# Kernel optimization log

Measured on AMD Instinct MI355X. Metric: run time of the kernel, lower is better.

## Reference

```python
import jax, jax.numpy as jnp
import numpy as np
from jax import lax

N_HEADS = 12
HEAD_DIM = 64
ALPHA = 4.0  # spikingjelly surrogate.Sigmoid default alpha
EPS = 1e-5   # BatchNorm1d default eps

@jax.custom_vjp
def _heaviside(v):
    return (v >= 0.0).astype(v.dtype)

def _heaviside_fwd(v):
    return _heaviside(v), v

def _heaviside_bwd(v, g):
    sg = jax.nn.sigmoid(ALPHA * v)
    return (g * ALPHA * sg * (1.0 - sg),)

_heaviside.defvjp(_heaviside_fwd, _heaviside_bwd)

def if_node(x):
    """Multi-step IFNode (v_threshold=1, hard reset to 0), scan over leading T dim."""
    def step(v, xt):
        v = v + xt                      # integrate
        s = _heaviside(v - 1.0)         # fire
        v = (1.0 - s) * v               # hard reset: spiked neurons -> 0
        return v, s
    _, spikes = lax.scan(step, jnp.zeros_like(x[0]), x)
    return spikes

def bn1d(x):
    """Fresh (training-mode) BatchNorm1d over (T, S, D) with channels=S;
    affine weight=1, bias=0 at init, so pure normalization over axes (0,2)."""
    mean = x.mean(axis=(0, 2), keepdims=True)
    var = x.var(axis=(0, 2), keepdims=True)  # biased variance, as torch BN uses
    return (x - mean) * lax.rsqrt(var + EPS)

def setup_inputs() -> dict:
    key = jax.random.key(0)
    ks = jax.random.split(key, 5)
    T, S, D = 4, 2048, 768
    x = jax.random.normal(ks[0], (T, S, D), dtype=jnp.float32)
    scale = 0.02
    wq = jax.random.normal(ks[1], (D, D), dtype=jnp.float32) * scale
    wk = jax.random.normal(ks[2], (D, D), dtype=jnp.float32) * scale
    wv = jax.random.normal(ks[3], (D, D), dtype=jnp.float32) * scale
    wo = jax.random.normal(ks[4], (D, D), dtype=jnp.float32) * scale
    return {"x": x, "wq": wq, "wk": wk, "wv": wv, "wo": wo, "cur_pos": S}

def reference(x, wq, wk, wv, wo, cur_pos):
    T, S, D = x.shape
    tmp = if_node(x)                    # init_spike
    Q = tmp @ wq
    V = tmp @ wv
    K = tmp @ wk
    Q = if_node(bn1d(Q))                # spike_q(bnq(Q))
    V = if_node(bn1d(V))                # spike_v(bnv(V))
    K = if_node(bn1d(K))                # spike_k(bnk(K))
    # (T, S, H, hd) -> (T, H, S, hd)
    Qh = Q.reshape(T, S, N_HEADS, HEAD_DIM).transpose(0, 2, 1, 3)
    Vh = V.reshape(T, S, N_HEADS, HEAD_DIM).transpose(0, 2, 1, 3)
    Kh = K.reshape(T, S, N_HEADS, HEAD_DIM).transpose(0, 2, 1, 3)
    QK = (Qh * Kh).sum(axis=2, keepdims=True)   # (T, H, 1, hd)
    QK = if_node(QK)                    # talking_heads
    QKV = Vh * QK                       # (T, H, S, hd)
    QKV = QKV.transpose(0, 2, 1, 3).reshape(T, S, D)
    return bn1d(QKV @ wo)
```

## Files before the change

kernel.cpp:

```cpp
#include <hip/hip_runtime.h>

#define T_ 4
#define S_ 2048
#define D_ 768
#define SD_ (S_ * D_)
#define TSD_ (T_ * SD_)
#define H_ 12
#define HD_ 64
#define PLANE_BYTES 2359296u

typedef int int32x4 __attribute__((ext_vector_type(4)));

__device__ __forceinline__ void cp16(unsigned char* lds, const unsigned char* g) {
    __builtin_amdgcn_global_load_lds(
        (const __attribute__((address_space(1))) unsigned int*)g,
        (__attribute__((address_space(3))) unsigned int*)lds, 16, 0, 0);
}

__device__ __forceinline__ size_t frag_addr(int m, int d) {
    return ((size_t)(m >> 4) * 12 + (d >> 6)) * 1024 +
           (size_t)(((d >> 4) & 3) * 256 + (m & 15) * 16 + (d & 15));
}

__global__ __launch_bounds__(256) void k_prep_all(const float* __restrict__ wq,
                                                  const float* __restrict__ wk,
                                                  const float* __restrict__ wv,
                                                  const float* __restrict__ wo,
                                                  const float* __restrict__ x,
                                                  unsigned char* __restrict__ Bp,
                                                  unsigned char* __restrict__ Sx,
                                                  unsigned int* __restrict__ QKp) {
    __shared__ unsigned char wl[4096];
    int tid = threadIdx.x;
    if (blockIdx.y < 4) {
        const float* W = (blockIdx.y == 0) ? wq : (blockIdx.y == 1) ? wk
                       : (blockIdx.y == 2) ? wv : wo;
        unsigned char* out = Bp + (size_t)blockIdx.y * PLANE_BYTES;
        int c = blockIdx.x;
        int kb = c % 12;
        int nbg = c / 12;
        int k_loc = tid >> 2;
        int n_base = (tid & 3) * 4;
        float4 w4 = *(const float4*)(
            W + (size_t)(kb * 64 + k_loc) * D_ + nbg * 16 + n_base);
        float wsv[4] = {w4.x, w4.y, w4.z, w4.w};
#pragma unroll
        for (int j = 0; j < 4; j++) {
            int n_loc = n_base + j;
            int u = (int)rintf(wsv[j] * 1073741824.0f);
#pragma unroll
            for (int p = 0; p < 4; p++) {
                wl[p * 1024 + (n_loc + 16 * (k_loc >> 4)) * 16 + (k_loc & 15)] =
                    (unsigned char)(u & 255);
                u = (u + 128) >> 8;
            }
        }
        __syncthreads();
        int p = tid >> 6;
        int lane = tid & 63;
        uint4 val = *(const uint4*)&wl[p * 1024 + lane * 16];
        *(uint4*)(out + (size_t)((p * 48 + nbg) * 12 + kb) * 1024 + lane * 16) =
            val;
    } else {
        if (blockIdx.x >= 384) {
            if (blockIdx.x < 432) {
                int idx = (blockIdx.x - 384) * 256 + tid;
                QKp[idx] = 0u;
            }
            return;
        }
        int gid = blockIdx.x * 256 + tid;
        int s = gid / 48;
        int d0 = (gid % 48) * 16;
        double v[16];
#pragma unroll
        for (int j = 0; j < 16; j++) v[j] = 0.0;
#pragma unroll
        for (int t = 0; t < T_; t++) {
            union { uint4 u; unsigned char b[16]; } sp;
#pragma unroll
            for (int q = 0; q < 4; q++) {
                float4 xt = *(const float4*)(
                    x + (size_t)t * SD_ + (size_t)s * D_ + d0 + q * 4);
                float xs[4] = {xt.x, xt.y, xt.z, xt.w};
#pragma unroll
                for (int j = 0; j < 4; j++) {
                    int jj = q * 4 + j;
                    v[jj] += (double)xs[j];
                    unsigned char ss = (v[jj] >= 1.0) ? 1 : 0;
                    sp.b[jj] = ss;
                    if (ss) v[jj] = 0.0;
                }
            }
            *(uint4*)(Sx + frag_addr(t * S_ + s, d0)) = sp.u;
        }
    }
}

#define GBUF 24576

__global__ __launch_bounds__(256, 2) void k_gemm_i8(
    const unsigned char* __restrict__ A,
    const unsigned char* __restrict__ Bp,
    const unsigned int* __restrict__ Mp,
    float* __restrict__ C0, float* __restrict__ C1, float* __restrict__ C2,
    int bzoff) {
    int z = blockIdx.z;
    const unsigned char* B = Bp + (size_t)(bzoff + z) * PLANE_BYTES;
    float* C = (z == 0) ? C0 : (z == 1) ? C1 : C2;

    __shared__ __align__(16) unsigned char lds[2 * GBUF];
    __shared__ __align__(16) unsigned int maskw[192];

    int tid = threadIdx.x;
    int lane = tid & 63;
    int w = tid >> 6;
    int wm = w >> 1;
    int wn = w & 1;
    int row0 = blockIdx.x * 128;
    int tI = row0 >> 11;
    int n0 = blockIdx.y * 64;
    int nbg0 = blockIdx.y * 4;
    int col = lane & 15;
    int quad = lane >> 4;

    const unsigned char* Ag = A + (size_t)(row0 >> 4) * 12 * 1024 + lane * 16;
    const unsigned char* Bg = B + lane * 16;

    auto stage = [&](int buf, int kb) {
        unsigned char* dst = lds + buf * GBUF;
#pragma unroll
        for (int i = 0; i < 2; i++) {
            int mc = w * 2 + i;
            cp16(dst + mc * 1024, Ag + (size_t)(mc * 12 + kb) * 1024);
        }
#pragma unroll
        for (int qi = 0; qi < 4; qi++) {
            int q = w * 4 + qi;
            int p = q >> 2;
            int nb = q & 3;
            cp16(dst + 8192 + q * 1024,
                 Bg + (size_t)((p * 48 + nbg0 + nb) * 12 + kb) * 1024);
        }
    };

    int32x4 zerov = {0, 0, 0, 0};
    int32x4 acc[4][2][4];
#pragma unroll
    for (int mb = 0; mb < 4; mb++)
#pragma unroll
        for (int nb = 0; nb < 2; nb++)
#pragma unroll
            for (int p = 0; p < 4; p++) acc[mb][nb][p] = zerov;

    stage(0, 0);
    stage(1, 1);
    if (Mp && tid < 192) {
        unsigned int m = 0;
#pragma unroll
        for (int c = 0; c < 16; c++) m |= Mp[c * 768 + tI * 192 + tid];
        maskw[tid] = m;
    }
    asm volatile("s_waitcnt vmcnt(0)" ::: "memory");
    __syncthreads();

    auto kstep = [&](int kb, int cur, bool dostage, bool last) {
        if (last) asm volatile("s_waitcnt vmcnt(0)" ::: "memory");
        else      asm volatile("s_waitcnt vmcnt(6)" ::: "memory");
        __builtin_amdgcn_sched_barrier(0);
        __builtin_amdgcn_s_barrier();
        asm volatile("" ::: "memory");
        __builtin_amdgcn_sched_barrier(0);
        const unsigned char* Ab = lds + cur * GBUF;
        const unsigned char* Bb = Ab + 8192;
        __builtin_amdgcn_s_setprio(1);
        int32x4 af[4];
#pragma unroll
        for (int mb = 0; mb < 4; mb++)
            af[mb] = *(const int32x4*)(Ab + (wm * 4 + mb) * 1024 + lane * 16);
        if (Mp) {
            int32x4 mv = *(const int32x4*)((const unsigned char*)maskw +
                                           kb * 64 + quad * 16);
#pragma unroll
            for (int mb = 0; mb < 4; mb++) af[mb] &= mv;
        }
#pragma unroll
        for (int p = 0; p < 4; p++)
#pragma unroll
            for (int nb = 0; nb < 2; nb++) {
                int32x4 bf = *(const int32x4*)(
                    Bb + (p * 4 + wn * 2 + nb) * 1024 + lane * 16);
#pragma unroll
                for (int mb = 0; mb < 4; mb++)
                    acc[mb][nb][p] = __builtin_amdgcn_mfma_i32_16x16x64_i8(
                        af[mb], bf, acc[mb][nb][p], 0, 0, 0);
            }
        __builtin_amdgcn_s_setprio(0);
        asm volatile("s_waitcnt lgkmcnt(0)" ::: "memory");
        __builtin_amdgcn_sched_barrier(0);
        __builtin_amdgcn_s_barrier();
        asm volatile("" ::: "memory");
        __builtin_amdgcn_sched_barrier(0);
        if (dostage) stage(cur, kb + 2);
    };

    for (int kb2 = 0; kb2 < 5; kb2++) {
        kstep(2 * kb2, 0, true, false);
        kstep(2 * kb2 + 1, 1, true, false);
    }
    kstep(10, 0, false, false);
    kstep(11, 1, false, true);

#pragma unroll
    for (int mb = 0; mb < 4; mb++)
#pragma unroll
        for (int nb = 0; nb < 2; nb++)
#pragma unroll
            for (int r = 0; r < 4; r++) {
                double td = (double)acc[mb][nb][0][r]
                          + 256.0 * (double)acc[mb][nb][1][r]
                          + 65536.0 * (double)acc[mb][nb][2][r]
                          + 16777216.0 * (double)acc[mb][nb][3][r];
                float v = (float)(td * (1.0 / 1073741824.0));
                int rr = row0 + wm * 64 + mb * 16 + quad * 4 + r;
                int cc = n0 + wn * 32 + nb * 16 + col;
                C[(size_t)rr * D_ + cc] = v;
            }
}

__global__ __launch_bounds__(256) void k_bnif_qk(const float* __restrict__ Qf,
                                                 const float* __restrict__ Kf,
                                                 const float* __restrict__ Vf,
                                                 unsigned char* __restrict__ Vs,
                                                 unsigned int* __restrict__ QKp) {
    int s = blockIdx.x;
    __shared__ float buf[3][T_][D_];
    __shared__ double red[4][6];
    __shared__ unsigned char spkV[T_ * D_];
    __shared__ unsigned char spkA[T_ * D_];
    __shared__ double stats[3][2];

    int tid = threadIdx.x;
    int lane = tid & 63, wv = tid >> 6;
    const float* Xs[3] = {Qf, Kf, Vf};
    double sum[3] = {0.0, 0.0, 0.0}, sumsq[3] = {0.0, 0.0, 0.0};
#pragma unroll
    for (int y = 0; y < 3; y++) {
#pragma unroll
        for (int i = 0; i < 3; i++) {
            int idx = i * 256 + tid;
            int t = idx / 192;
            int c = idx - t * 192;
            float4 v = *(const float4*)(
                Xs[y] + (size_t)t * SD_ + (size_t)s * D_ + c * 4);
            *(float4*)&buf[y][t][c * 4] = v;
            sum[y] += ((double)v.x + (double)v.y) +
                      ((double)v.z + (double)v.w);
            sumsq[y] += ((double)v.x * v.x + (double)v.y * v.y) +
                        ((double)v.z * v.z + (double)v.w * v.w);
        }
    }
#pragma unroll
    for (int off = 32; off > 0; off >>= 1) {
#pragma unroll
        for (int y = 0; y < 3; y++) {
            sum[y] += __shfl_down(sum[y], off);
            sumsq[y] += __shfl_down(sumsq[y], off);
        }
    }
    if (lane == 0) {
#pragma unroll
        for (int y = 0; y < 3; y++) {
            red[wv][y] = sum[y];
            red[wv][3 + y] = sumsq[y];
        }
    }
    __syncthreads();
    if (tid < 3) {
        double s4 = red[0][tid] + red[1][tid] + red[2][tid] + red[3][tid];
        double q4 = red[0][3 + tid] + red[1][3 + tid] + red[2][3 + tid] +
                    red[3][3 + tid];
        double mean = s4 / 3072.0;
        double var = q4 / 3072.0 - mean * mean;
        stats[tid][0] = mean;
        stats[tid][1] = 1.0 / sqrt(var + 1e-5);
    }
    __syncthreads();

    for (int d = tid; d < D_; d += 256) {
        unsigned char qs[T_], ks[T_];
#pragma unroll
        for (int y = 0; y < 3; y++) {
            double mean = stats[y][0], rstd = stats[y][1];
            double v = 0.0;
#pragma unroll
            for (int t = 0; t < T_; t++) {
                double xn = ((double)buf[y][t][d] - mean) * rstd;
                v += xn;
                unsigned char sp = (v >= 1.0) ? 1 : 0;
                if (y == 0) qs[t] = sp;
                else if (y == 1) ks[t] = sp;
                else spkV[t * D_ + d] = sp;
                if (sp) v = 0.0;
            }
        }
#pragma unroll
        for (int t = 0; t < T_; t++) spkA[t * D_ + d] = qs[t] & ks[t];
    }
    __syncthreads();

    if (tid < 192) {
        int tt = tid / 48, gg = tid % 48;
        uint4 val = *(const uint4*)&spkV[tt * D_ + gg * 16];
        size_t dst = ((size_t)(tt * 128 + (s >> 4)) * 12 + (gg >> 2)) * 1024 +
                     (size_t)((gg & 3) * 256 + (s & 15) * 16);
        *(uint4*)(Vs + dst) = val;
        unsigned int* dstq = QKp + (s & 15) * 768;
#pragma unroll
        for (int t = 0; t < T_; t++) {
            unsigned int word = *(const unsigned int*)&spkA[t * D_ + tid * 4];
            if (word) atomicOr(dstq + t * 192 + tid, word);
        }
    }
}

__global__ __launch_bounds__(256) void k_bn_out(const float* __restrict__ Xin,
                                                float* __restrict__ out) {
    int s = blockIdx.x;
    __shared__ double red[4][2];
    __shared__ double st[2];
    int tid = threadIdx.x;
    int lane = tid & 63, wv = tid >> 6;
    float4 vv[3];
    double sum = 0.0, sumsq = 0.0;
#pragma unroll
    for (int i = 0; i < 3; i++) {
        int idx = i * 256 + tid;
        int t = idx / 192, c = idx - t * 192;
        float4 v = *(const float4*)(
            Xin + (size_t)t * SD_ + (size_t)s * D_ + c * 4);
        vv[i] = v;
        sum += ((double)v.x + (double)v.y) + ((double)v.z + (double)v.w);
        sumsq += ((double)v.x * v.x + (double)v.y * v.y) +
                 ((double)v.z * v.z + (double)v.w * v.w);
    }
#pragma unroll
    for (int off = 32; off > 0; off >>= 1) {
        sum += __shfl_down(sum, off);
        sumsq += __shfl_down(sumsq, off);
    }
    if (lane == 0) { red[wv][0] = sum; red[wv][1] = sumsq; }
    __syncthreads();
    if (tid == 0) {
        double s4 = red[0][0] + red[1][0] + red[2][0] + red[3][0];
        double q4 = red[0][1] + red[1][1] + red[2][1] + red[3][1];
        double mean = s4 / 3072.0;
        double var = q4 / 3072.0 - mean * mean;
        st[0] = mean;
        st[1] = 1.0 / sqrt(var + 1e-5);
    }
    __syncthreads();
    double mean = st[0], rstd = st[1];
#pragma unroll
    for (int i = 0; i < 3; i++) {
        int idx = i * 256 + tid;
        int t = idx / 192, c = idx - t * 192;
        float4 o;
        o.x = (float)(((double)vv[i].x - mean) * rstd);
        o.y = (float)(((double)vv[i].y - mean) * rstd);
        o.z = (float)(((double)vv[i].z - mean) * rstd);
        o.w = (float)(((double)vv[i].w - mean) * rstd);
        *(float4*)(out + (size_t)t * SD_ + (size_t)s * D_ + c * 4) = o;
    }
}

extern "C" void kernel_launch(void* const* d_in, const int* in_sizes, int n_in,
                              void* d_out, int out_size, void* d_ws,
                              size_t ws_size, hipStream_t stream) {
    const float* x  = (const float*)d_in[0];
    const float* wq = (const float*)d_in[1];
    const float* wk = (const float*)d_in[2];
    const float* wv = (const float*)d_in[3];
    const float* wo = (const float*)d_in[4];
    float* out = (float*)d_out;

    float* ws  = (float*)d_ws;
    float* Qf  = ws;
    float* Kf  = ws + (size_t)TSD_;
    float* Vf  = ws + (size_t)2 * TSD_;
    unsigned int* QKp = (unsigned int*)(ws + (size_t)3 * TSD_);
    unsigned char* Sx = (unsigned char*)(QKp + 12288);
    unsigned char* Vs = Sx + (size_t)TSD_;
    unsigned char* Bp = Vs + (size_t)TSD_;

    k_prep_all<<<dim3(576, 5), 256, 0, stream>>>(wq, wk, wv, wo, x, Bp, Sx,
                                                 QKp);
    k_gemm_i8<<<dim3(64, 12, 3), 256, 0, stream>>>(Sx, Bp, nullptr,
                                                   Qf, Kf, Vf, 0);
    k_bnif_qk<<<S_, 256, 0, stream>>>(Qf, Kf, Vf, Vs, QKp);
    k_gemm_i8<<<dim3(64, 12, 1), 256, 0, stream>>>(Vs, Bp, QKp, Qf, Qf, Qf, 3);
    k_bn_out<<<S_, 256, 0, stream>>>(Qf, out);
}
```

Before: 230.6 us.

## Load A fragments directly to registers and stage only B through LDS

The int8 GEMM no longer stages the A tile through LDS. Each wave now loads its A fragments straight from global memory into registers, double-buffered one k-block ahead. B is staged two k-blocks at a time into 32KB double buffers, which halves the number of barriers per k-loop and drops the explicit waitcnt/setprio scheduling. The LDS footprint grows to 64KB, which could limit occupancy with two blocks per CU, and the direct global A loads may expose latency.

```diff
diff --git a/kernel.cpp b/kernel.cpp
--- a/kernel.cpp
+++ b/kernel.cpp
@@ -97,8 +97,6 @@
     }
 }
 
-#define GBUF 24576
-
 __global__ __launch_bounds__(256, 2) void k_gemm_i8(
     const unsigned char* __restrict__ A,
     const unsigned char* __restrict__ Bp,
@@ -109,7 +107,7 @@
     const unsigned char* B = Bp + (size_t)(bzoff + z) * PLANE_BYTES;
     float* C = (z == 0) ? C0 : (z == 1) ? C1 : C2;
 
-    __shared__ __align__(16) unsigned char lds[2 * GBUF];
+    __shared__ __align__(16) unsigned char bsm[2 * 32768];
     __shared__ __align__(16) unsigned int maskw[192];
 
     int tid = threadIdx.x;
@@ -124,26 +122,6 @@
     int col = lane & 15;
     int quad = lane >> 4;
 
-    const unsigned char* Ag = A + (size_t)(row0 >> 4) * 12 * 1024 + lane * 16;
-    const unsigned char* Bg = B + lane * 16;
-
-    auto stage = [&](int buf, int kb) {
-        unsigned char* dst = lds + buf * GBUF;
-#pragma unroll
-        for (int i = 0; i < 2; i++) {
-            int mc = w * 2 + i;
-            cp16(dst + mc * 1024, Ag + (size_t)(mc * 12 + kb) * 1024);
-        }
-#pragma unroll
-        for (int qi = 0; qi < 4; qi++) {
-            int q = w * 4 + qi;
-            int p = q >> 2;
-            int nb = q & 3;
-            cp16(dst + 8192 + q * 1024,
-                 Bg + (size_t)((p * 48 + nbg0 + nb) * 12 + kb) * 1024);
-        }
-    };
-
     int32x4 zerov = {0, 0, 0, 0};
     int32x4 acc[4][2][4];
 #pragma unroll
@@ -153,63 +131,72 @@
 #pragma unroll
             for (int p = 0; p < 4; p++) acc[mb][nb][p] = zerov;
 
-    stage(0, 0);
-    stage(1, 1);
+    const unsigned char* Ab =
+        A + (size_t)((row0 >> 4) + wm * 4) * 12 * 1024 + lane * 16;
+
+    auto stageB = [&](int buf, int kb2) {
+        unsigned char* bb = bsm + buf * 32768;
+#pragma unroll
+        for (int kk = 0; kk < 2; kk++)
+#pragma unroll
+            for (int qi = 0; qi < 4; qi++) {
+                int q = w * 4 + qi;
+                int p = q >> 2, nb = q & 3;
+                cp16(bb + kk * 16384 + q * 1024,
+                     B + (size_t)((p * 48 + nbg0 + nb) * 12 + 2 * kb2 + kk) *
+                             1024 + lane * 16);
+            }
+    };
+
+    stageB(0, 0);
     if (Mp && tid < 192) {
         unsigned int m = 0;
 #pragma unroll
         for (int c = 0; c < 16; c++) m |= Mp[c * 768 + tI * 192 + tid];
         maskw[tid] = m;
     }
-    asm volatile("s_waitcnt vmcnt(0)" ::: "memory");
-    __syncthreads();
-
-    auto kstep = [&](int kb, int cur, bool dostage, bool last) {
-        if (last) asm volatile("s_waitcnt vmcnt(0)" ::: "memory");
-        else      asm volatile("s_waitcnt vmcnt(6)" ::: "memory");
-        __builtin_amdgcn_sched_barrier(0);
-        __builtin_amdgcn_s_barrier();
-        asm volatile("" ::: "memory");
-        __builtin_amdgcn_sched_barrier(0);
-        const unsigned char* Ab = lds + cur * GBUF;
-        const unsigned char* Bb = Ab + 8192;
-        __builtin_amdgcn_s_setprio(1);
-        int32x4 af[4];
-#pragma unroll
-        for (int mb = 0; mb < 4; mb++)
-            af[mb] = *(const int32x4*)(Ab + (wm * 4 + mb) * 1024 + lane * 16);
-        if (Mp) {
-            int32x4 mv = *(const int32x4*)((const unsigned char*)maskw +
-                                           kb * 64 + quad * 16);
-#pragma unroll
-            for (int mb = 0; mb < 4; mb++) af[mb] &= mv;
-        }
-#pragma unroll
-        for (int p = 0; p < 4; p++)
-#pragma unroll
-            for (int nb = 0; nb < 2; nb++) {
-                int32x4 bf = *(const int32x4*)(
-                    Bb + (p * 4 + wn * 2 + nb) * 1024 + lane * 16);
+    int32x4 a[2][4];
+#pragma unroll
+    for (int mb = 0; mb < 4; mb++)
+        a[0][mb] = *(const int32x4*)(Ab + (size_t)(mb * 12) * 1024);
+    __syncthreads();
+
+    for (int kb2 = 0; kb2 < 6; kb2++) {
+        int cur = kb2 & 1;
+        if (kb2 < 5) stageB(1 - cur, kb2 + 1);
+#pragma unroll
+        for (int kbh = 0; kbh < 2; kbh++) {
+            int kb = kb2 * 2 + kbh;
+            if (kb < 11) {
 #pragma unroll
                 for (int mb = 0; mb < 4; mb++)
-                    acc[mb][nb][p] = __builtin_amdgcn_mfma_i32_16x16x64_i8(
-                        af[mb], bf, acc[mb][nb][p], 0, 0, 0);
-            }
-        __builtin_amdgcn_s_setprio(0);
-        asm volatile("s_waitcnt lgkmcnt(0)" ::: "memory");
-        __builtin_amdgcn_sched_barrier(0);
-        __builtin_amdgcn_s_barrier();
-        asm volatile("" ::: "memory");
-        __builtin_amdgcn_sched_barrier(0);
-        if (dostage) stage(cur, kb + 2);
-    };
-
-    for (int kb2 = 0; kb2 < 5; kb2++) {
-        kstep(2 * kb2, 0, true, false);
-        kstep(2 * kb2 + 1, 1, true, false);
-    }
-    kstep(10, 0, false, false);
-    kstep(11, 1, false, true);
+                    a[(kb + 1) & 1][mb] = *(const int32x4*)(
+                        Ab + (size_t)(mb * 12 + kb + 1) * 1024);
+            }
+            int32x4 af[4];
+#pragma unroll
+            for (int mb = 0; mb < 4; mb++) af[mb] = a[kb & 1][mb];
+            if (Mp) {
+                int32x4 mv = *(const int32x4*)(
+                    (const unsigned char*)maskw + kb * 64 + quad * 16);
+#pragma unroll
+                for (int mb = 0; mb < 4; mb++) af[mb] &= mv;
+            }
+            const unsigned char* bb = bsm + cur * 32768 + kbh * 16384;
+#pragma unroll
+            for (int p = 0; p < 4; p++)
+#pragma unroll
+                for (int nb = 0; nb < 2; nb++) {
+                    int32x4 bf = *(const int32x4*)(
+                        bb + (size_t)(p * 4 + wn * 2 + nb) * 1024 + lane * 16);
+#pragma unroll
+                    for (int mb = 0; mb < 4; mb++)
+                        acc[mb][nb][p] = __builtin_amdgcn_mfma_i32_16x16x64_i8(
+                            af[mb], bf, acc[mb][nb][p], 0, 0, 0);
+                }
+        }
+        __syncthreads();
+    }
 
 #pragma unroll
     for (int mb = 0; mb < 4; mb++)
```

New measurement: 200.0 us, median of 2. 13.2% less time.
